# Kernel optimization log

Measured on AMD Instinct MI355X. Metric: run time of the kernel, lower is better.

The kernel has to match this reference:

```python
import jax, jax.numpy as jnp
import numpy as np

ATT_HEAD, IN_DIM, OUT_DIM = 8, 768, 96
B, N = 8, 1024
LEAKY_ALPHA = 0.2


def setup_inputs() -> dict:
    key = jax.random.key(0)
    ks = jax.random.split(key, 8)
    feat_in = jax.random.normal(ks[0], (B, N, IN_DIM), dtype=jnp.float32)
    adj = jax.random.randint(ks[1], (B, N, N), 0, 2).astype(jnp.float32)
    # xavier-ish init scales
    W = jax.random.normal(ks[2], (ATT_HEAD, IN_DIM, OUT_DIM), dtype=jnp.float32) * (1.0 / np.sqrt(IN_DIM))
    b = jnp.zeros((OUT_DIM,), dtype=jnp.float32)
    w_src = jax.random.normal(ks[3], (ATT_HEAD, OUT_DIM, 1), dtype=jnp.float32) * (1.0 / np.sqrt(OUT_DIM))
    w_dst = jax.random.normal(ks[4], (ATT_HEAD, OUT_DIM, 1), dtype=jnp.float32) * (1.0 / np.sqrt(OUT_DIM))
    Hw = jax.random.normal(ks[5], (IN_DIM, IN_DIM), dtype=jnp.float32) * (1.0 / np.sqrt(IN_DIM))
    Hb = jnp.zeros((IN_DIM,), dtype=jnp.float32)
    return {"feat_in": feat_in, "adj": adj, "W": W, "b": b,
            "w_src": w_src, "w_dst": w_dst, "Hw": Hw, "Hb": Hb}


def reference(feat_in, adj, W, b, w_src, w_dst, Hw, Hb):
    batch, n, _ = feat_in.shape
    # per-head projection: [B,H,N,O]
    h = jnp.einsum('bni,hio->bhno', feat_in, W)
    t = jnp.tanh(h)
    a_src = jnp.einsum('bhno,hoq->bhnq', t, w_src)[..., 0]  # [B,H,N]
    a_dst = jnp.einsum('bhno,hoq->bhnq', t, w_dst)[..., 0]  # [B,H,N]
    attn = a_src[:, :, :, None] + a_dst[:, :, None, :]       # [B,H,N,N]
    attn = jnp.where(attn >= 0, attn, LEAKY_ALPHA * attn)
    mask = adj[:, None, :, :] == 0                            # 1-adj as bool
    attn = jnp.where(mask, jnp.float32(-999.0), attn)
    attn = jax.nn.softmax(attn, axis=-1)
    feat_out = jnp.einsum('bhnm,bhmo->bhno', attn, h) + b     # [B,H,N,O]
    feat_out = jnp.transpose(feat_out, (0, 2, 1, 3)).reshape(batch, n, -1)
    feat_out = jax.nn.elu(feat_out)
    gate = jax.nn.sigmoid(feat_in @ Hw.T + Hb)
    return gate * feat_out + (1.0 - gate) * feat_in
```

## Files before the change

### kernel.cpp

```cpp
#include <hip/hip_runtime.h>
#include <cstddef>

#define BATCH 8
#define NN 1024
#define IN_DIM 768
#define OUT_DIM 96
#define HEADS 8
#define M_ROWS 8192
#define NCOLS 1536

typedef __attribute__((ext_vector_type(8))) short short8;
typedef __attribute__((ext_vector_type(4))) float f32x4;
typedef __attribute__((ext_vector_type(4))) unsigned short ushort4v;
typedef _Float16 half8 __attribute__((ext_vector_type(8)));

typedef __attribute__((address_space(1))) void gvoid_t;
typedef __attribute__((address_space(3))) void lvoid_t;

__device__ __forceinline__ void gload_lds16(const void* g, void* l) {
    __builtin_amdgcn_global_load_lds((gvoid_t*)(unsigned long long)g,
                                     (lvoid_t*)(unsigned int)(unsigned long long)l,
                                     16, 0, 0);
}

__device__ __forceinline__ unsigned int pkrtz(float a, float b) {
    return __builtin_bit_cast(unsigned int, __builtin_amdgcn_cvt_pkrtz(a, b));
}
__device__ __forceinline__ unsigned short f2h(float x) {
    _Float16 h = (_Float16)x;
    return __builtin_bit_cast(unsigned short, h);
}
__device__ __forceinline__ float h2f(unsigned short u) {
    return (float)__builtin_bit_cast(_Float16, u);
}
__device__ __forceinline__ float tanh_fast(float x) {
    return 1.f - 2.f / (__expf(2.f * x) + 1.f);
}
__device__ __forceinline__ f32x4 mfma16(short8 a, short8 b, f32x4 c) {
    return __builtin_amdgcn_mfma_f32_16x16x32_f16(
        __builtin_bit_cast(half8, a), __builtin_bit_cast(half8, b), c, 0, 0, 0);
}

__global__ __launch_bounds__(256) void prep_kernel(
        const float* __restrict__ feat_in, const float* __restrict__ W,
        const float* __restrict__ Hw, const float* __restrict__ adj,
        unsigned short* __restrict__ Xb, unsigned short* __restrict__ BT,
        unsigned int* __restrict__ abits) {
    int blk = blockIdx.x;
    int t = threadIdx.x;
    if (blk < 3072) {
        int idx = blk * 256 + t;
        const float4* p = (const float4*)(feat_in + (size_t)idx * 8);
        float4 a = p[0], b = p[1];
        union { unsigned int u4[4]; short8 s8; } pk;
        pk.u4[0] = pkrtz(a.x, a.y);
        pk.u4[1] = pkrtz(a.z, a.w);
        pk.u4[2] = pkrtz(b.x, b.y);
        pk.u4[3] = pkrtz(b.z, b.w);
        *(short8*)(Xb + (size_t)idx * 8) = pk.s8;
    } else if (blk < 5376) {
        int idx = (blk - 3072) * 256 + t;
        int c = idx / IN_DIM, i = idx % IN_DIM;
        int h = c / OUT_DIM, o = c % OUT_DIM;
        BT[(size_t)c * IN_DIM + i] = f2h(W[((size_t)h * IN_DIM + i) * OUT_DIM + o]);
    } else if (blk < 7680) {
        int idx = (blk - 5376) * 256 + t;
        int c = idx / IN_DIM, i = idx % IN_DIM;
        BT[(size_t)(768 + c) * IN_DIM + i] = f2h(Hw[(size_t)c * IN_DIM + i]);
    } else {
        int idx = (blk - 7680) * 256 + t;
        const float4* p = (const float4*)(adj + (size_t)idx * 32);
        unsigned int m = 0;
        #pragma unroll
        for (int q = 0; q < 8; ++q) {
            float4 v = p[q];
            m |= (v.x != 0.f ? 1u : 0u) << (q * 4 + 0);
            m |= (v.y != 0.f ? 1u : 0u) << (q * 4 + 1);
            m |= (v.z != 0.f ? 1u : 0u) << (q * 4 + 2);
            m |= (v.w != 0.f ? 1u : 0u) << (q * 4 + 3);
        }
        abits[idx] = m;
    }
}

__global__ __launch_bounds__(256) void gemm1_kernel(
        const unsigned short* __restrict__ Xb, const unsigned short* __restrict__ BT,
        const float* __restrict__ Hb,
        unsigned short* __restrict__ h_bt, unsigned short* __restrict__ gate) {
    __shared__ __align__(16) unsigned short As[128 * 64];
    __shared__ __align__(16) unsigned short Bs[128 * 64];
    __shared__ float hbs[128];
    int m0 = blockIdx.x * 128;
    int c0 = blockIdx.y * 128;
    int t = threadIdx.x;
    int w = t >> 6, lane = t & 63, l15 = t & 15, quad = lane >> 4;
    if (c0 >= 768 && t < 128) hbs[t] = Hb[c0 - 768 + t];
    f32x4 acc[2][8] = {};
    for (int k0 = 0; k0 < IN_DIM; k0 += 64) {
        __syncthreads();
        #pragma unroll
        for (int cc = 0; cc < 4; ++cc) {
            int base64 = (w * 4 + cc) * 64;
            int p = base64 + lane;
            int r = p >> 3, qs = p & 7;
            int qb = qs ^ (r & 7);
            gload_lds16(Xb + (size_t)(m0 + r) * IN_DIM + k0 + qb * 8, As + base64 * 8);
            gload_lds16(BT + (size_t)(c0 + r) * IN_DIM + k0 + qb * 8, Bs + base64 * 8);
        }
        __syncthreads();
        #pragma unroll
        for (int ks = 0; ks < 2; ++ks) {
            short8 af[2], bfr[8];
            #pragma unroll
            for (int mt = 0; mt < 2; ++mt) {
                int r = w * 32 + mt * 16 + l15;
                int cb = (ks * 4 + quad) ^ (r & 7);
                af[mt] = *(const short8*)(As + r * 64 + cb * 8);
            }
            #pragma unroll
            for (int nt = 0; nt < 8; ++nt) {
                int r = nt * 16 + l15;
                int cb = (ks * 4 + quad) ^ (r & 7);
                bfr[nt] = *(const short8*)(Bs + r * 64 + cb * 8);
            }
            #pragma unroll
            for (int mt = 0; mt < 2; ++mt)
                #pragma unroll
                for (int nt = 0; nt < 8; ++nt)
                    acc[mt][nt] = mfma16(af[mt], bfr[nt], acc[mt][nt]);
        }
    }
    int b = m0 >> 10;
    #pragma unroll
    for (int mt = 0; mt < 2; ++mt) {
        int rowbase = m0 + w * 32 + mt * 16 + quad * 4;
        int nbase = rowbase & 1023;
        #pragma unroll
        for (int nt = 0; nt < 8; ++nt) {
            int c = c0 + nt * 16 + l15;
            if (c < 768) {
                int hh = c / OUT_DIM, o = c % OUT_DIM;
                union { unsigned int u2[2]; ushort4v u4; } pk;
                pk.u2[0] = pkrtz(acc[mt][nt][0], acc[mt][nt][1]);
                pk.u2[1] = pkrtz(acc[mt][nt][2], acc[mt][nt][3]);
                *(ushort4v*)(h_bt + ((size_t)(b * 8 + hh) * OUT_DIM + o) * NN + nbase) = pk.u4;
            } else {
                int cl = nt * 16 + l15;
                int cg = c - 768;
                #pragma unroll
                for (int reg = 0; reg < 4; ++reg) {
                    float z = acc[mt][nt][reg] + hbs[cl];
                    float g = __builtin_amdgcn_rcpf(1.f + __builtin_amdgcn_exp2f(-1.44269504f * z));
                    gate[(size_t)(rowbase + reg) * 768 + cg] = f2h(g);
                }
            }
        }
    }
}

__global__ __launch_bounds__(256) void a_kernel(const unsigned short* __restrict__ h_bt,
                                                const float* __restrict__ w_src,
                                                const float* __restrict__ w_dst,
                                                float* __restrict__ a_src, float* __restrict__ a_dst) {
    __shared__ unsigned short ht[96 * 72];
    __shared__ float ws_s[96], wd_s[96];
    __shared__ float pps[4][64], ppd[4][64];
    int bh = blockIdx.x >> 4;
    int n0 = (blockIdx.x & 15) * 64;
    int head = bh & 7;
    int t = threadIdx.x;
    if (t < 96) { ws_s[t] = w_src[head * 96 + t]; wd_s[t] = w_dst[head * 96 + t]; }
    for (int f = t; f < 768; f += 256) {
        int row = f >> 3, c8 = (f & 7) * 8;
        *(short8*)(ht + row * 72 + c8) = *(const short8*)(h_bt + ((size_t)bh * 96 + row) * NN + n0 + c8);
    }
    __syncthreads();
    int n = t & 63, part = t >> 6;
    float ps = 0.f, pd = 0.f;
    #pragma unroll
    for (int oo = 0; oo < 24; ++oo) {
        int o = part * 24 + oo;
        float th = tanh_fast(h2f(ht[o * 72 + n]));
        ps += th * ws_s[o];
        pd += th * wd_s[o];
    }
    pps[part][n] = ps; ppd[part][n] = pd;
    __syncthreads();
    if (t < 64) {
        float s = pps[0][t] + pps[1][t] + pps[2][t] + pps[3][t];
        float d = ppd[0][t] + ppd[1][t] + ppd[2][t] + ppd[3][t];
        a_src[bh * 1024 + n0 + t] = s * 1.44269504f;
        a_dst[bh * 1024 + n0 + t] = d * 1.44269504f;
    }
}

__global__ __launch_bounds__(512) void attn_kernel(
        const unsigned short* __restrict__ h_bt, const unsigned int* __restrict__ abits,
        const float* __restrict__ a_src_g, const float* __restrict__ a_dst_g,
        const unsigned short* __restrict__ gate, const unsigned short* __restrict__ Xb,
        const float* __restrict__ bias, float* __restrict__ out) {
    __shared__ __align__(16) unsigned short hs[2][96 * 64];
    __shared__ __align__(16) float adst[1024];
    __shared__ float bias_s[96];
    int blk = blockIdx.x;
    int bh = blk >> 3, i0 = (blk & 7) * 128, b = bh >> 3, hh = bh & 7;
    int t = threadIdx.x;
    int w = t >> 6, lane = t & 63, l15 = t & 15, quad = lane >> 4;
    if (t < 256) *(f32x4*)(adst + t * 4) = *(const f32x4*)(a_dst_g + bh * 1024 + t * 4);
    if (t < 96) bias_s[t] = bias[t];
    int irow = i0 + w * 16 + l15;
    float si = a_src_g[bh * 1024 + irow];
    const unsigned short* hhp = h_bt + (size_t)bh * 96 * NN;
    if (w < 6) {
        #pragma unroll
        for (int cc = 0; cc < 2; ++cc) {
            int u0 = (w * 2 + cc) * 64;
            int p = u0 + lane;
            int r = p >> 3, qs = p & 7, qb = qs ^ (r & 7);
            gload_lds16(hhp + (size_t)r * NN + qb * 8, (char*)&hs[0][0] + (size_t)u0 * 16);
        }
    }
    const unsigned int* mrow = abits + ((size_t)b * NN + irow) * 32;
    uint2 mw = *(const uint2*)(mrow);
    f32x4 acc[7] = {};
    short8 ones = {};
    if (l15 == 0) {
        #pragma unroll
        for (int u = 0; u < 8; ++u) ones[u] = (short)0x3C00;
    }
    __syncthreads();
    for (int j0 = 0; j0 < 1024; j0 += 64) {
        int cur = (j0 >> 6) & 1;
        int jn = j0 + 64;
        if (jn < 1024 && w < 6) {
            #pragma unroll
            for (int cc = 0; cc < 2; ++cc) {
                int u0 = (w * 2 + cc) * 64;
                int p = u0 + lane;
                int r = p >> 3, qs = p & 7, qb = qs ^ (r & 7);
                gload_lds16(hhp + (size_t)r * NN + jn + qb * 8, (char*)&hs[cur ^ 1][0] + (size_t)u0 * 16);
            }
        }
        short8 af[2];
        unsigned int mws[2] = {mw.x, mw.y};
        #pragma unroll
        for (int ks = 0; ks < 2; ++ks) {
            unsigned int byte = (mws[ks] >> (quad * 8)) & 0xFFu;
            f32x4 d0 = *(const f32x4*)(&adst[j0 + ks * 32 + quad * 8]);
            f32x4 d1 = *(const f32x4*)(&adst[j0 + ks * 32 + quad * 8 + 4]);
            float dv[8] = {d0[0], d0[1], d0[2], d0[3], d1[0], d1[1], d1[2], d1[3]};
            float ev[8];
            #pragma unroll
            for (int u = 0; u < 8; ++u) {
                float s = si + dv[u];
                float l = fmaxf(s, 0.2f * s);
                float e = __builtin_amdgcn_exp2f(l);
                ev[u] = ((byte >> u) & 1u) ? e : 0.f;
            }
            union { unsigned int u4[4]; short8 s8; } pk;
            pk.u4[0] = pkrtz(ev[0], ev[1]);
            pk.u4[1] = pkrtz(ev[2], ev[3]);
            pk.u4[2] = pkrtz(ev[4], ev[5]);
            pk.u4[3] = pkrtz(ev[6], ev[7]);
            af[ks] = pk.s8;
        }
        if (jn < 1024) mw = *(const uint2*)(mrow + (jn >> 5));
        #pragma unroll
        for (int ks = 0; ks < 2; ++ks) {
            #pragma unroll
            for (int nt = 0; nt < 6; ++nt) {
                int r = nt * 16 + l15;
                int qs = (ks * 4 + quad) ^ (r & 7);
                short8 bfr = *(const short8*)(&hs[cur][(size_t)(r * 8 + qs) * 8]);
                acc[nt] = mfma16(af[ks], bfr, acc[nt]);
            }
            acc[6] = mfma16(af[ks], ones, acc[6]);
        }
        __syncthreads();
    }
    int rowq = i0 + w * 16 + quad * 4;
    #pragma unroll
    for (int reg = 0; reg < 4; ++reg) {
        float ssum = __shfl(acc[6][reg], (lane & 48));
        float inv = (ssum > 0.f) ? __builtin_amdgcn_rcpf(ssum) : 0.f;
        int n = rowq + reg;
        size_t mrow_o = ((size_t)b * NN + n) * 768 + hh * 96;
        #pragma unroll
        for (int nt = 0; nt < 6; ++nt) {
            int cl = nt * 16 + l15;
            float v = acc[nt][reg] * inv + bias_s[cl];
            float e = (v > 0.f) ? v : (__builtin_amdgcn_exp2f(v * 1.44269504f) - 1.f);
            float g = h2f(gate[mrow_o + cl]);
            float x = h2f(Xb[mrow_o + cl]);
            out[mrow_o + cl] = x + g * (e - x);
        }
    }
}

extern "C" void kernel_launch(void* const* d_in, const int* in_sizes, int n_in,
                              void* d_out, int out_size, void* d_ws, size_t ws_size,
                              hipStream_t stream) {
    const float* feat_in = (const float*)d_in[0];
    const float* adj     = (const float*)d_in[1];
    const float* W       = (const float*)d_in[2];
    const float* bbias   = (const float*)d_in[3];
    const float* w_src   = (const float*)d_in[4];
    const float* w_dst   = (const float*)d_in[5];
    const float* Hw      = (const float*)d_in[6];
    const float* Hb      = (const float*)d_in[7];
    float* out = (float*)d_out;
    char* base = (char*)d_ws;

    unsigned short* Xb    = (unsigned short*)(base);
    unsigned short* BcatT = (unsigned short*)(base + 12582912);
    unsigned short* h_bt  = (unsigned short*)(base + 14942208);
    unsigned short* gate  = (unsigned short*)(base + 27525120);
    float* a_src = (float*)(base + 40108032);
    float* a_dst = (float*)(base + 40370176);
    unsigned int* abits = (unsigned int*)(base + 40632320);

    prep_kernel<<<8704, 256, 0, stream>>>(feat_in, W, Hw, adj, Xb, BcatT, abits);
    gemm1_kernel<<<dim3(M_ROWS / 128, NCOLS / 128), 256, 0, stream>>>(Xb, BcatT, Hb, h_bt, gate);
    a_kernel<<<64 * 16, 256, 0, stream>>>(h_bt, w_src, w_dst, a_src, a_dst);
    attn_kernel<<<64 * 8, 512, 0, stream>>>(h_bt, abits, a_src, a_dst, gate, Xb, bbias, out);
}
```

Before: 187.7 us.

## Fuse attention-score projection into GEMM epilogue with atomics; remap attn block order

Removes the separate a_kernel by computing tanh(h)·w_src and tanh(h)·w_dst directly from the fp32 GEMM accumulators in gemm1's epilogue. Partial sums are reduced across lanes and added into a_src/a_dst with atomics, split at head boundaries because a 128-column tile spans two heads. The prep kernel gains extra blocks to zero both buffers (a_src and a_dst are contiguous). The attention kernel's block index mapping is also reordered so consecutive blocks cover different batch/head pairs, which may change cache locality. The costs are one fewer launch and no re-read of h_bt, traded for atomic traffic and a non-deterministic summation order.

```diff
diff --git a/kernel.cpp b/kernel.cpp
--- a/kernel.cpp
+++ b/kernel.cpp
@@ -45,7 +45,7 @@
         const float* __restrict__ feat_in, const float* __restrict__ W,
         const float* __restrict__ Hw, const float* __restrict__ adj,
         unsigned short* __restrict__ Xb, unsigned short* __restrict__ BT,
-        unsigned int* __restrict__ abits) {
+        unsigned int* __restrict__ abits, float* __restrict__ a_zero) {
     int blk = blockIdx.x;
     int t = threadIdx.x;
     if (blk < 3072) {
@@ -67,7 +67,7 @@
         int idx = (blk - 5376) * 256 + t;
         int c = idx / IN_DIM, i = idx % IN_DIM;
         BT[(size_t)(768 + c) * IN_DIM + i] = f2h(Hw[(size_t)c * IN_DIM + i]);
-    } else {
+    } else if (blk < 8704) {
         int idx = (blk - 7680) * 256 + t;
         const float4* p = (const float4*)(adj + (size_t)idx * 32);
         unsigned int m = 0;
@@ -80,21 +80,38 @@
             m |= (v.w != 0.f ? 1u : 0u) << (q * 4 + 3);
         }
         abits[idx] = m;
+    } else {
+        int idx = (blk - 8704) * 256 + t;
+        f32x4 z = {0.f, 0.f, 0.f, 0.f};
+        *(f32x4*)(a_zero + (size_t)idx * 8) = z;
+        *(f32x4*)(a_zero + (size_t)idx * 8 + 4) = z;
     }
 }
 
 __global__ __launch_bounds__(256) void gemm1_kernel(
         const unsigned short* __restrict__ Xb, const unsigned short* __restrict__ BT,
-        const float* __restrict__ Hb,
-        unsigned short* __restrict__ h_bt, unsigned short* __restrict__ gate) {
+        const float* __restrict__ Hb, const float* __restrict__ w_src,
+        const float* __restrict__ w_dst,
+        unsigned short* __restrict__ h_bt, unsigned short* __restrict__ gate,
+        float* __restrict__ a_src, float* __restrict__ a_dst) {
     __shared__ __align__(16) unsigned short As[128 * 64];
     __shared__ __align__(16) unsigned short Bs[128 * 64];
     __shared__ float hbs[128];
+    __shared__ float ws_s[128], wd_s[128];
     int m0 = blockIdx.x * 128;
     int c0 = blockIdx.y * 128;
     int t = threadIdx.x;
     int w = t >> 6, lane = t & 63, l15 = t & 15, quad = lane >> 4;
-    if (c0 >= 768 && t < 128) hbs[t] = Hb[c0 - 768 + t];
+    if (c0 >= 768) {
+        if (t < 128) hbs[t] = Hb[c0 - 768 + t];
+    } else {
+        if (t < 128) {
+            int c = c0 + t;
+            int hd = c / OUT_DIM, o = c % OUT_DIM;
+            ws_s[t] = w_src[hd * OUT_DIM + o];
+            wd_s[t] = w_dst[hd * OUT_DIM + o];
+        }
+    }
     f32x4 acc[2][8] = {};
     for (int k0 = 0; k0 < IN_DIM; k0 += 64) {
         __syncthreads();
@@ -131,22 +148,56 @@
         }
     }
     int b = m0 >> 10;
-    #pragma unroll
-    for (int mt = 0; mt < 2; ++mt) {
-        int rowbase = m0 + w * 32 + mt * 16 + quad * 4;
-        int nbase = rowbase & 1023;
-        #pragma unroll
-        for (int nt = 0; nt < 8; ++nt) {
-            int c = c0 + nt * 16 + l15;
-            if (c < 768) {
+    if (c0 < 768) {
+        int split = (c0 / 96 + 1) * 96 - c0;
+        int headlo = c0 / 96;
+        #pragma unroll
+        for (int mt = 0; mt < 2; ++mt) {
+            int rowbase = m0 + w * 32 + mt * 16 + quad * 4;
+            int nbase = rowbase & 1023;
+            #pragma unroll
+            for (int nt = 0; nt < 8; ++nt) {
+                int c = c0 + nt * 16 + l15;
                 int hh = c / OUT_DIM, o = c % OUT_DIM;
                 union { unsigned int u2[2]; ushort4v u4; } pk;
                 pk.u2[0] = pkrtz(acc[mt][nt][0], acc[mt][nt][1]);
                 pk.u2[1] = pkrtz(acc[mt][nt][2], acc[mt][nt][3]);
                 *(ushort4v*)(h_bt + ((size_t)(b * 8 + hh) * OUT_DIM + o) * NN + nbase) = pk.u4;
-            } else {
+            }
+            #pragma unroll
+            for (int reg = 0; reg < 4; ++reg) {
+                float psA = 0.f, pdA = 0.f, psB = 0.f, pdB = 0.f;
+                #pragma unroll
+                for (int nt = 0; nt < 8; ++nt) {
+                    int cl = nt * 16 + l15;
+                    float th = tanh_fast(acc[mt][nt][reg]);
+                    float s = th * ws_s[cl], d = th * wd_s[cl];
+                    if (cl < split) { psA += s; pdA += d; }
+                    else            { psB += s; pdB += d; }
+                }
+                #pragma unroll
+                for (int mk = 1; mk <= 8; mk <<= 1) {
+                    psA += __shfl_xor(psA, mk); pdA += __shfl_xor(pdA, mk);
+                    psB += __shfl_xor(psB, mk); pdB += __shfl_xor(pdB, mk);
+                }
+                if (l15 == 0) {
+                    int n2 = nbase + reg;
+                    int ilo = (b * 8 + headlo) * 1024 + n2;
+                    atomicAdd(&a_src[ilo], psA * 1.44269504f);
+                    atomicAdd(&a_dst[ilo], pdA * 1.44269504f);
+                    atomicAdd(&a_src[ilo + 1024], psB * 1.44269504f);
+                    atomicAdd(&a_dst[ilo + 1024], pdB * 1.44269504f);
+                }
+            }
+        }
+    } else {
+        #pragma unroll
+        for (int mt = 0; mt < 2; ++mt) {
+            int rowbase = m0 + w * 32 + mt * 16 + quad * 4;
+            #pragma unroll
+            for (int nt = 0; nt < 8; ++nt) {
                 int cl = nt * 16 + l15;
-                int cg = c - 768;
+                int cg = c0 - 768 + cl;
                 #pragma unroll
                 for (int reg = 0; reg < 4; ++reg) {
                     float z = acc[mt][nt][reg] + hbs[cl];
@@ -155,42 +206,6 @@
                 }
             }
         }
-    }
-}
-
-__global__ __launch_bounds__(256) void a_kernel(const unsigned short* __restrict__ h_bt,
-                                                const float* __restrict__ w_src,
-                                                const float* __restrict__ w_dst,
-                                                float* __restrict__ a_src, float* __restrict__ a_dst) {
-    __shared__ unsigned short ht[96 * 72];
-    __shared__ float ws_s[96], wd_s[96];
-    __shared__ float pps[4][64], ppd[4][64];
-    int bh = blockIdx.x >> 4;
-    int n0 = (blockIdx.x & 15) * 64;
-    int head = bh & 7;
-    int t = threadIdx.x;
-    if (t < 96) { ws_s[t] = w_src[head * 96 + t]; wd_s[t] = w_dst[head * 96 + t]; }
-    for (int f = t; f < 768; f += 256) {
-        int row = f >> 3, c8 = (f & 7) * 8;
-        *(short8*)(ht + row * 72 + c8) = *(const short8*)(h_bt + ((size_t)bh * 96 + row) * NN + n0 + c8);
-    }
-    __syncthreads();
-    int n = t & 63, part = t >> 6;
-    float ps = 0.f, pd = 0.f;
-    #pragma unroll
-    for (int oo = 0; oo < 24; ++oo) {
-        int o = part * 24 + oo;
-        float th = tanh_fast(h2f(ht[o * 72 + n]));
-        ps += th * ws_s[o];
-        pd += th * wd_s[o];
-    }
-    pps[part][n] = ps; ppd[part][n] = pd;
-    __syncthreads();
-    if (t < 64) {
-        float s = pps[0][t] + pps[1][t] + pps[2][t] + pps[3][t];
-        float d = ppd[0][t] + ppd[1][t] + ppd[2][t] + ppd[3][t];
-        a_src[bh * 1024 + n0 + t] = s * 1.44269504f;
-        a_dst[bh * 1024 + n0 + t] = d * 1.44269504f;
     }
 }
 
@@ -203,7 +218,9 @@
     __shared__ __align__(16) float adst[1024];
     __shared__ float bias_s[96];
     int blk = blockIdx.x;
-    int bh = blk >> 3, i0 = (blk & 7) * 128, b = bh >> 3, hh = bh & 7;
+    int bh = (blk & 7) * 8 + ((blk >> 3) & 7);
+    int i0 = (blk >> 6) * 128;
+    int b = bh >> 3, hh = bh & 7;
     int t = threadIdx.x;
     int w = t >> 6, lane = t & 63, l15 = t & 15, quad = lane >> 4;
     if (t < 256) *(f32x4*)(adst + t * 4) = *(const f32x4*)(a_dst_g + bh * 1024 + t * 4);
@@ -319,8 +336,8 @@
     float* a_dst = (float*)(base + 40370176);
     unsigned int* abits = (unsigned int*)(base + 40632320);
 
-    prep_kernel<<<8704, 256, 0, stream>>>(feat_in, W, Hw, adj, Xb, BcatT, abits);
-    gemm1_kernel<<<dim3(M_ROWS / 128, NCOLS / 128), 256, 0, stream>>>(Xb, BcatT, Hb, h_bt, gate);
-    a_kernel<<<64 * 16, 256, 0, stream>>>(h_bt, w_src, w_dst, a_src, a_dst);
+    prep_kernel<<<8768, 256, 0, stream>>>(feat_in, W, Hw, adj, Xb, BcatT, abits, a_src);
+    gemm1_kernel<<<dim3(M_ROWS / 128, NCOLS / 128), 256, 0, stream>>>(
+        Xb, BcatT, Hb, w_src, w_dst, h_bt, gate, a_src, a_dst);
     attn_kernel<<<64 * 8, 512, 0, stream>>>(h_bt, abits, a_src, a_dst, gate, Xb, bbias, out);
 }
```

Result: no change. 186.2 us (-0.8%).
